# Performance work log

Measured on AMD Instinct MI355X. Metric: run time of the kernel, lower is better.

## Reference

```python
import jax, jax.numpy as jnp
import numpy as np

L = 2      # dec_num_layer
B = 32     # batch_size
T = 128    # block_len
H = 128    # dec_num_unit
F = 3      # code_rate_n / code_rate_k
D = 10


def _gru_cell(x, h, Wih, Whh, bih, bhh):
    # PyTorch GRU gate order: r, z, n
    gx = x @ Wih.T + bih
    gh = h @ Whh.T + bhh
    rx, zx, nx = jnp.split(gx, 3, axis=-1)
    rh, zh, nh = jnp.split(gh, 3, axis=-1)
    r = jax.nn.sigmoid(rx + rh)
    z = jax.nn.sigmoid(zx + zh)
    n = jnp.tanh(nx + r * nh)
    return (1.0 - z) * n + z * h


def _gru_stack(x, h, params):
    # x: [B, F], h: [L, B, H]; params: list of (Wih, Whh, bih, bhh) per layer
    hs = []
    inp = x
    for l, (Wih, Whh, bih, bhh) in enumerate(params):
        hl = _gru_cell(inp, h[l], Wih, Whh, bih, bhh)
        hs.append(hl)
        inp = hl
    return jnp.stack(hs), inp  # new hidden [L,B,H], top-layer output [B,H]


def _attend(h_raw, hist, i, attn_W, v_W, fc2_W, fc2_b):
    # h_raw: [L,B,H]; hist: [L,B,T,H]; growing-context attention with mask t<=i
    Ws, Wh = attn_W[:, :H], attn_W[:, H:]
    e = jnp.tanh((h_raw @ Ws.T)[:, :, None, :] + hist @ Wh.T)   # [L,B,T,H]
    logits = jnp.einsum('lbth,h->lbt', e, v_W[0])               # [L,B,T]
    mask = jnp.arange(T) <= i
    logits = jnp.where(mask[None, None, :], logits, -jnp.inf)
    a = jax.nn.softmax(logits, axis=-1)
    c = jnp.einsum('lbt,lbth->lbh', a, hist)                    # [L,B,H]
    return jnp.concatenate([c, h_raw], axis=-1) @ fc2_W.T + fc2_b


def _forward(received, params1, params2, attn_W, v_W, fc2_W, fc2_b, out_W, out_b):
    xs_seq = jnp.transpose(received, (1, 0, 2))  # [T,B,F]

    def step(carry, xs):
        h1, h2, hist1, hist2 = carry
        i, x = xs
        h1_raw, out1 = _gru_stack(x, h1, params1)
        h2_raw, out2 = _gru_stack(x, h2, params2)
        hist1 = hist1.at[:, :, i, :].set(h1_raw)
        hist2 = hist2.at[:, :, i, :].set(h2_raw)
        h1_att = _attend(h1_raw, hist1, i, attn_W, v_W, fc2_W, fc2_b)
        h2_att = _attend(h2_raw, hist2, i, attn_W, v_W, fc2_W, fc2_b)
        # torch skips the attention/fc2 update at step 0
        h1n = jnp.where(i > 0, h1_att, h1_raw)
        h2n = jnp.where(i > 0, h2_att, h2_raw)
        return (h1n, h2n, hist1, hist2), (out1, out2)

    z = jnp.zeros((L, B, H), dtype=received.dtype)
    zh = jnp.zeros((L, B, T, H), dtype=received.dtype)
    _, (o1, o2) = jax.lax.scan(step, (z, z, zh, zh), (jnp.arange(T), xs_seq))
    rnn1 = jnp.transpose(o1, (1, 0, 2))  # [B,T,H]
    rnn2 = jnp.transpose(o2, (1, 0, 2))

    idx = jnp.minimum(jnp.arange(T) + D, T - 1)
    rt_d = rnn2[:, idx, :]
    rnn_out = jnp.concatenate([rnn1, rt_d], axis=-1)            # [B,T,2H]
    dec = jnp.tanh(rnn_out @ out_W.T + out_b)                   # dec_act = tanh
    return jax.nn.sigmoid(dec)                                  # [B,T,1]


def setup_inputs() -> dict:
    key = jax.random.key(0)
    ks = iter(jax.random.split(key, 64))
    s = 0.05
    d = {"received": jax.random.normal(next(ks), (B, T, F), dtype=jnp.float32)}
    for dec in (1, 2):
        for l in range(L):
            inp = F if l == 0 else H
            d[f"Wih{dec}_{l}"] = jax.random.normal(next(ks), (3 * H, inp), dtype=jnp.float32) * s
            d[f"Whh{dec}_{l}"] = jax.random.normal(next(ks), (3 * H, H), dtype=jnp.float32) * s
            d[f"bih{dec}_{l}"] = jax.random.normal(next(ks), (3 * H,), dtype=jnp.float32) * s
            d[f"bhh{dec}_{l}"] = jax.random.normal(next(ks), (3 * H,), dtype=jnp.float32) * s
    d["attn_W"] = jax.random.normal(next(ks), (H, 2 * H), dtype=jnp.float32) * s
    d["v_W"] = jax.random.normal(next(ks), (1, H), dtype=jnp.float32) * s
    d["fc2_W"] = jax.random.normal(next(ks), (H, 2 * H), dtype=jnp.float32) * s
    d["fc2_b"] = jax.random.normal(next(ks), (H,), dtype=jnp.float32) * s
    d["out_W"] = jax.random.normal(next(ks), (1, 2 * H), dtype=jnp.float32) * s
    d["out_b"] = jax.random.normal(next(ks), (1,), dtype=jnp.float32) * s
    return d


def reference(received,
              Wih1_0, Whh1_0, bih1_0, bhh1_0, Wih1_1, Whh1_1, bih1_1, bhh1_1,
              Wih2_0, Whh2_0, bih2_0, bhh2_0, Wih2_1, Whh2_1, bih2_1, bhh2_1,
              attn_W, v_W, fc2_W, fc2_b, out_W, out_b):
    params1 = [(Wih1_0, Whh1_0, bih1_0, bhh1_0), (Wih1_1, Whh1_1, bih1_1, bhh1_1)]
    params2 = [(Wih2_0, Whh2_0, bih2_0, bhh2_0), (Wih2_1, Whh2_1, bih2_1, bhh2_1)]
    return _forward(received, params1, params2, attn_W, v_W, fc2_W, fc2_b, out_W, out_b)
```

## Files before the change

### kernel.cpp

```cpp
#include <hip/hip_runtime.h>

typedef _Float16 half_t;
typedef __attribute__((ext_vector_type(2))) _Float16 half2_t;

__device__ __forceinline__ half2_t bc2(unsigned int u){ return __builtin_bit_cast(half2_t, u); }
__device__ __forceinline__ int   bcI(half2_t v){ return __builtin_bit_cast(int, v); }
__device__ __forceinline__ half2_t bcH(int v){ return __builtin_bit_cast(half2_t, v); }
__device__ __forceinline__ float fdot2f(half2_t a, half2_t b, float c){
  return __builtin_amdgcn_fdot2(a, b, c, false);
}
__device__ __forceinline__ float rcp_f(float x){ return __builtin_amdgcn_rcpf(x); }
__device__ __forceinline__ float sigmoidf_(float x){ return rcp_f(1.0f+__expf(-x)); }
__device__ __forceinline__ float tanhf_(float x){ return 1.0f - 2.0f*rcp_f(__expf(2.0f*x)+1.0f); }

__device__ __forceinline__ float qxor1(float v){
  return __builtin_bit_cast(float, __builtin_amdgcn_mov_dpp(__builtin_bit_cast(int,v),0xB1,0xF,0xF,true));
}
__device__ __forceinline__ float qxor2(float v){
  return __builtin_bit_cast(float, __builtin_amdgcn_mov_dpp(__builtin_bit_cast(int,v),0x4E,0xF,0xF,true));
}
__device__ __forceinline__ float qsum4(float v){ v += qxor1(v); v += qxor2(v); return v; }

__device__ __forceinline__ void bar(){
  asm volatile("s_waitcnt lgkmcnt(0)\n\ts_barrier" ::: "memory");
}

__device__ __forceinline__ float dot32(const uint4* w, const uint4* x){
  float a=0.f,b=0.f,c=0.f,d=0.f;
  #pragma unroll
  for (int m=0;m<4;++m){
    a=fdot2f(bc2(w[m].x),bc2(x[m].x),a);
    b=fdot2f(bc2(w[m].y),bc2(x[m].y),b);
    c=fdot2f(bc2(w[m].z),bc2(x[m].z),c);
    d=fdot2f(bc2(w[m].w),bc2(x[m].w),d);
  }
  return (a+b)+(c+d);
}

__global__ void pack_k(const float* __restrict__ src, half_t* __restrict__ dst,
                       int R, int K, int ld, int coloff, int RT, int row_off){
  int idx = blockIdx.x*blockDim.x + threadIdx.x;
  if (idx >= R*K) return;
  int r = idx / K, k = idx - r*K;
  int kc = k >> 3, j = k & 7;
  dst[((size_t)kc*RT + row_off + r)*8 + j] = (half_t)src[(size_t)r*ld + coloff + k];
}

__launch_bounds__(512)
__global__ void gru_main(
    const float* __restrict__ received,
    const float* __restrict__ Wih0d0, const float* __restrict__ Wih0d1,
    const float* __restrict__ bx0d0, const float* __restrict__ bh0d0,
    const float* __restrict__ bx1d0, const float* __restrict__ bh1d0,
    const float* __restrict__ bx0d1, const float* __restrict__ bh0d1,
    const float* __restrict__ bx1d1, const float* __restrict__ bh1d1,
    const float* __restrict__ vW, const float* __restrict__ fc2b,
    const half_t* __restrict__ W0pack, const half_t* __restrict__ W1pack,
    const half_t* __restrict__ WsPack, const half_t* __restrict__ WhPack,
    const half_t* __restrict__ fc2Pack,
    half_t* __restrict__ o1h, half_t* __restrict__ o2h)
{
  const int dec = blockIdx.x >> 5;
  const int b   = blockIdx.x & 31;
  const int tid = threadIdx.x;
  const int q   = tid & 3;
  const int r   = tid >> 2;

  const float* bx0  = dec ? bx0d1 : bx0d0;
  const float* bh0  = dec ? bh0d1 : bh0d0;
  const float* bx1  = dec ? bx1d1 : bx1d0;
  const float* bh1  = dec ? bh1d1 : bh1d0;
  const float* Wih0 = dec ? Wih0d1 : Wih0d0;
  const half_t* W0  = W0pack + (size_t)dec*49152;
  const half_t* W1  = W1pack + (size_t)dec*98304;
  half_t* od = dec ? o2h : o1h;

  __shared__ __align__(16) half_t sh_hist[2][128*136];
  __shared__ __align__(16) half_t sh_histWh[2][128*136];
  __shared__ __align__(16) float  sh_gx[384];
  __shared__ __align__(16) float  sh_gh[384];
  __shared__ __align__(16) float  sh_g1x[384];
  __shared__ __align__(16) float  sh_g1h[384];
  __shared__ __align__(16) half_t sh_sWs16[2][128];
  __shared__ __align__(16) float  sh_probs[2][128];
  __shared__ __align__(16) float  sh_hatt32[2][128];
  __shared__ __align__(16) half_t sh_hatt_pk[2][128];
  __shared__ __align__(16) float  sh_hraw32[2][128];
  __shared__ __align__(16) half_t sh_hraw_pk[2][128];
  __shared__ __align__(16) half_t sh_fc2in[2][256];
  __shared__ __align__(16) half_t sh_vW16[128];

  float bA=0.f,bB=0.f,bC=0.f;
  if (q==0){ bA=bh0[r];     bB=bh1[r+128]; bC=bx1[r];     }
  else if (q==1){ bA=bh0[r+128]; bB=bh1[r+256]; bC=bx1[r+128]; }
  else if (q==2){ bA=bh0[r+256];                bC=bx1[r+256]; }
  else { bB=bh1[r]; }
  const float bF = fc2b[r];
  float wx0=0.f,wx1=0.f,wx2=0.f,wxw=0.f;
  if (tid < 384){ wx0=Wih0[tid*3]; wx1=Wih0[tid*3+1]; wx2=Wih0[tid*3+2]; wxw=bx0[tid]; }

  {
    uint4 z = make_uint4(0u,0u,0u,0u);
    uint4* ph = reinterpret_cast<uint4*>(&sh_hist[0][0]);
    uint4* pw = reinterpret_cast<uint4*>(&sh_histWh[0][0]);
    for (int j=tid; j<4352; j+=512){ ph[j]=z; pw[j]=z; }
  }
  if (tid < 256){ int l=tid>>7, rr=tid&127; sh_hatt32[l][rr]=0.f; sh_hatt_pk[l][rr]=(half_t)0.f; }
  if (tid < 128) sh_vW16[tid] = (half_t)vW[tid];
  bar();

  for (int i=0; i<128; ++i){
    {
      uint4 xa[4];
      #pragma unroll
      for (int m=0;m<4;++m) xa[m] = *reinterpret_cast<const uint4*>(&sh_hatt_pk[0][32*q+8*m]);
      float a0,a1,a2;
      {
        uint4 w[12];
        #pragma unroll
        for (int n=0;n<3;++n)
          #pragma unroll
          for (int m=0;m<4;++m)
            w[4*n+m] = *reinterpret_cast<const uint4*>(W0 + ((size_t)(4*q+m)*384 + r + 128*n)*8);
        a0 = dot32(&w[0],xa); a1 = dot32(&w[4],xa); a2 = dot32(&w[8],xa);
      }
      uint4 xb[4];
      #pragma unroll
      for (int m=0;m<4;++m) xb[m] = *reinterpret_cast<const uint4*>(&sh_hatt_pk[1][32*q+8*m]);
      float a3,a4,a5;
      {
        uint4 w[12];
        #pragma unroll
        for (int n=0;n<3;++n)
          #pragma unroll
          for (int m=0;m<4;++m)
            w[4*n+m] = *reinterpret_cast<const uint4*>(W1 + ((size_t)(4*q+m)*768 + 384 + r + 128*n)*8);
        a3 = dot32(&w[0],xb); a4 = dot32(&w[4],xb); a5 = dot32(&w[8],xb);
      }
      a0=qsum4(a0); a1=qsum4(a1); a2=qsum4(a2);
      a3=qsum4(a3); a4=qsum4(a4); a5=qsum4(a5);
      if      (q==0){ sh_gh[r]      = a0+bA; sh_g1h[r+128] = a4+bB; }
      else if (q==1){ sh_gh[r+128]  = a1+bA; sh_g1h[r+256] = a5+bB; }
      else if (q==2){ sh_gh[r+256]  = a2+bA; }
      else          { sh_g1h[r]     = a3+bB; }
      if (tid < 384){
        const float* xr = &received[((size_t)b*128+i)*3];
        sh_gx[tid] = wxw + wx0*xr[0] + wx1*xr[1] + wx2*xr[2];
      }
    }
    bar();
    if (tid < 128){
      float rr = sigmoidf_(sh_gx[tid]+sh_gh[tid]);
      float zz = sigmoidf_(sh_gx[128+tid]+sh_gh[128+tid]);
      float nn = tanhf_(sh_gx[256+tid] + rr*sh_gh[256+tid]);
      float h0 = (1.f-zz)*nn + zz*sh_hatt32[0][tid];
      sh_hraw32[0][tid]=h0;
      half_t hh=(half_t)h0;
      sh_hist[0][i*136 + ((tid>>3)^(i&15))*8 + (tid&7)] = hh;
      sh_hraw_pk[0][tid]=hh; sh_fc2in[0][128+tid]=hh;
    }
    bar();
    {
      uint4 xc[4];
      #pragma unroll
      for (int m=0;m<4;++m) xc[m] = *reinterpret_cast<const uint4*>(&sh_hraw_pk[0][32*q+8*m]);
      uint4 w[12];
      #pragma unroll
      for (int n=0;n<3;++n)
        #pragma unroll
        for (int m=0;m<4;++m)
          w[4*n+m] = *reinterpret_cast<const uint4*>(W1 + ((size_t)(4*q+m)*768 + r + 128*n)*8);
      float a0 = dot32(&w[0],xc), a1 = dot32(&w[4],xc), a2 = dot32(&w[8],xc);
      a0=qsum4(a0); a1=qsum4(a1); a2=qsum4(a2);
      if      (q==0) sh_g1x[r]     = a0+bC;
      else if (q==1) sh_g1x[r+128] = a1+bC;
      else if (q==2) sh_g1x[r+256] = a2+bC;
    }
    bar();
    if (tid < 128){
      float rr = sigmoidf_(sh_g1x[tid]+sh_g1h[tid]);
      float zz = sigmoidf_(sh_g1x[128+tid]+sh_g1h[128+tid]);
      float nn = tanhf_(sh_g1x[256+tid] + rr*sh_g1h[256+tid]);
      float h1 = (1.f-zz)*nn + zz*sh_hatt32[1][tid];
      sh_hraw32[1][tid]=h1;
      half_t hh=(half_t)h1;
      sh_hist[1][i*136 + ((tid>>3)^(i&15))*8 + (tid&7)] = hh;
      sh_hraw_pk[1][tid]=hh; sh_fc2in[1][128+tid]=hh;
      od[(size_t)(b*128+i)*128 + tid] = hh;
    }
    bar();
    {
      uint4 xa[4], xb[4], ws[4], wh[4];
      #pragma unroll
      for (int m=0;m<4;++m){
        xa[m] = *reinterpret_cast<const uint4*>(&sh_hraw_pk[0][32*q+8*m]);
        xb[m] = *reinterpret_cast<const uint4*>(&sh_hraw_pk[1][32*q+8*m]);
        ws[m] = *reinterpret_cast<const uint4*>(WsPack + ((size_t)(4*q+m)*128 + r)*8);
        wh[m] = *reinterpret_cast<const uint4*>(WhPack + ((size_t)(4*q+m)*128 + r)*8);
      }
      float sA0=qsum4(dot32(ws,xa));
      float sA1=qsum4(dot32(ws,xb));
      float sB0=qsum4(dot32(wh,xa));
      float sB1=qsum4(dot32(wh,xb));
      int phys = i*136 + ((r>>3)^(i&15))*8 + (r&7);
      if      (q==0) sh_sWs16[0][r] = (half_t)sA0;
      else if (q==1) sh_sWs16[1][r] = (half_t)sA1;
      else if (q==2) sh_histWh[0][phys] = (half_t)sB0;
      else           sh_histWh[1][phys] = (half_t)sB1;
    }
    bar();
    if (i > 0){
      {
        int h6=tid&1, t6=(tid>>1)&127, l6=tid>>8;
        if (t6 <= i){
          const half_t* hwrow = &sh_histWh[l6][t6*136];
          const half_t* swrow = &sh_sWs16[l6][64*h6];
          const half_t* vwrow = &sh_vW16[64*h6];
          int key = t6 & 15;
          float s = 0.f;
          #pragma unroll
          for (int m=0;m<8;++m){
            uint4 hw = *reinterpret_cast<const uint4*>(hwrow + (((8*h6+m)^key)*8));
            uint4 sw = *reinterpret_cast<const uint4*>(swrow + 8*m);
            uint4 vw = *reinterpret_cast<const uint4*>(vwrow + 8*m);
            half2_t h2,s2,v2;
            h2=bc2(hw.x); s2=bc2(sw.x); v2=bc2(vw.x);
            s += tanhf_((float)s2[0]+(float)h2[0])*(float)v2[0];
            s += tanhf_((float)s2[1]+(float)h2[1])*(float)v2[1];
            h2=bc2(hw.y); s2=bc2(sw.y); v2=bc2(vw.y);
            s += tanhf_((float)s2[0]+(float)h2[0])*(float)v2[0];
            s += tanhf_((float)s2[1]+(float)h2[1])*(float)v2[1];
            h2=bc2(hw.z); s2=bc2(sw.z); v2=bc2(vw.z);
            s += tanhf_((float)s2[0]+(float)h2[0])*(float)v2[0];
            s += tanhf_((float)s2[1]+(float)h2[1])*(float)v2[1];
            h2=bc2(hw.w); s2=bc2(sw.w); v2=bc2(vw.w);
            s += tanhf_((float)s2[0]+(float)h2[0])*(float)v2[0];
            s += tanhf_((float)s2[1]+(float)h2[1])*(float)v2[1];
          }
          s += qxor1(s);
          if (h6==0) sh_probs[l6][t6] = __expf(s - 4.0f);
        } else if ((tid&1)==0){
          sh_probs[tid>>8][(tid>>1)&127] = 0.f;
        }
      }
      bar();
      {
        int ts=tid&15, oc=(tid>>4)&15, l8=tid>>8;
        float c0=0.f,c1=0.f,c2=0.f,c3=0.f,c4=0.f,c5=0.f,c6=0.f,c7=0.f, ps=0.f;
        #pragma unroll
        for (int k=0;k<8;++k){
          int t = ts + 16*k;
          float p = sh_probs[l8][t];
          uint4 hv = *reinterpret_cast<const uint4*>(&sh_hist[l8][t*136 + ((oc^(t&15))*8)]);
          half2_t a=bc2(hv.x), e=bc2(hv.y), f=bc2(hv.z), g=bc2(hv.w);
          c0+=p*(float)a[0]; c1+=p*(float)a[1]; c2+=p*(float)e[0]; c3+=p*(float)e[1];
          c4+=p*(float)f[0]; c5+=p*(float)f[1]; c6+=p*(float)g[0]; c7+=p*(float)g[1];
          ps+=p;
        }
        c0+=qxor1(c0); c0+=qxor2(c0);  c1+=qxor1(c1); c1+=qxor2(c1);
        c2+=qxor1(c2); c2+=qxor2(c2);  c3+=qxor1(c3); c3+=qxor2(c3);
        c4+=qxor1(c4); c4+=qxor2(c4);  c5+=qxor1(c5); c5+=qxor2(c5);
        c6+=qxor1(c6); c6+=qxor2(c6);  c7+=qxor1(c7); c7+=qxor2(c7);
        ps+=qxor1(ps); ps+=qxor2(ps);
        half2_t p01={(half_t)c0,(half_t)c1}, p23={(half_t)c2,(half_t)c3};
        half2_t p45={(half_t)c4,(half_t)c5}, p67={(half_t)c6,(half_t)c7};
        p01 = p01 + bcH(__shfl_xor(bcI(p01),4)); p23 = p23 + bcH(__shfl_xor(bcI(p23),4));
        p45 = p45 + bcH(__shfl_xor(bcI(p45),4)); p67 = p67 + bcH(__shfl_xor(bcI(p67),4));
        ps += __shfl_xor(ps,4);
        p01 = p01 + bcH(__shfl_xor(bcI(p01),8)); p23 = p23 + bcH(__shfl_xor(bcI(p23),8));
        p45 = p45 + bcH(__shfl_xor(bcI(p45),8)); p67 = p67 + bcH(__shfl_xor(bcI(p67),8));
        ps += __shfl_xor(ps,8);
        if (ts==0){
          float inv = rcp_f(ps);
          half2_t o01={(half_t)((float)p01[0]*inv),(half_t)((float)p01[1]*inv)};
          half2_t o23={(half_t)((float)p23[0]*inv),(half_t)((float)p23[1]*inv)};
          half2_t o45={(half_t)((float)p45[0]*inv),(half_t)((float)p45[1]*inv)};
          half2_t o67={(half_t)((float)p67[0]*inv),(half_t)((float)p67[1]*inv)};
          *reinterpret_cast<uint4*>(&sh_fc2in[l8][oc*8]) =
              make_uint4((unsigned)bcI(o01),(unsigned)bcI(o23),(unsigned)bcI(o45),(unsigned)bcI(o67));
        }
      }
      bar();
      {
        float e0=0.f, e1=0.f;
        #pragma unroll
        for (int h=0; h<2; ++h){
          uint4 w[4], x0[4], x1[4];
          #pragma unroll
          for (int m=0;m<4;++m){
            int kc = 8*q + 4*h + m;
            w[m]  = *reinterpret_cast<const uint4*>(fc2Pack + ((size_t)kc*128 + r)*8);
            x0[m] = *reinterpret_cast<const uint4*>(&sh_fc2in[0][64*q + 32*h + 8*m]);
            x1[m] = *reinterpret_cast<const uint4*>(&sh_fc2in[1][64*q + 32*h + 8*m]);
          }
          e0 += dot32(w,x0);
          e1 += dot32(w,x1);
        }
        e0 = qsum4(e0); e1 = qsum4(e1);
        if      (q==0){ float v=e0+bF; sh_hatt32[0][r]=v; sh_hatt_pk[0][r]=(half_t)v; }
        else if (q==1){ float v=e1+bF; sh_hatt32[1][r]=v; sh_hatt_pk[1][r]=(half_t)v; }
      }
    } else {
      if (tid < 256){
        int l=tid>>7, row=tid&127;
        float hv = sh_hraw32[l][row];
        sh_hatt32[l][row]=hv; sh_hatt_pk[l][row]=(half_t)hv;
      }
    }
    bar();
  }
}

__global__ void out_kernel(const half_t* __restrict__ o1h, const half_t* __restrict__ o2h,
                           const float* __restrict__ outW, const float* __restrict__ outb,
                           float* __restrict__ dout){
  int tid = blockIdx.x*blockDim.x + threadIdx.x;
  int q = tid&3, job = tid>>2;
  int b = job>>7, t = job&127;
  int t2 = t+10; if (t2>127) t2=127;
  const half_t* r1 = o1h + (size_t)(b*128+t)*128;
  const half_t* r2 = o2h + (size_t)(b*128+t2)*128;
  float acc=0.f;
  for (int j=q*32; j<q*32+32; ++j) acc += outW[j]*(float)r1[j];
  for (int j=q*32; j<q*32+32; ++j) acc += outW[128+j]*(float)r2[j];
  acc += __shfl_xor(acc,1);
  acc += __shfl_xor(acc,2);
  if (q==0){
    float d = tanhf_(acc + outb[0]);
    dout[job] = rcp_f(1.f+__expf(-d));
  }
}

static inline void launch_pack(const void* src, half_t* dst, int R, int K, int ld,
                               int coloff, int RT, int row_off, hipStream_t s){
  int total = R*K;
  pack_k<<<(total+255)/256, 256, 0, s>>>((const float*)src, dst, R, K, ld, coloff, RT, row_off);
}

extern "C" void kernel_launch(void* const* d_in, const int* in_sizes, int n_in,
                              void* d_out, int out_size, void* d_ws, size_t ws_size,
                              hipStream_t stream) {
  const float* received = (const float*)d_in[0];
  const float* Wih1_0 = (const float*)d_in[1];
  const float* Whh1_0 = (const float*)d_in[2];
  const float* bih1_0 = (const float*)d_in[3];
  const float* bhh1_0 = (const float*)d_in[4];
  const float* Wih1_1 = (const float*)d_in[5];
  const float* Whh1_1 = (const float*)d_in[6];
  const float* bih1_1 = (const float*)d_in[7];
  const float* bhh1_1 = (const float*)d_in[8];
  const float* Wih2_0 = (const float*)d_in[9];
  const float* Whh2_0 = (const float*)d_in[10];
  const float* bih2_0 = (const float*)d_in[11];
  const float* bhh2_0 = (const float*)d_in[12];
  const float* Wih2_1 = (const float*)d_in[13];
  const float* Whh2_1 = (const float*)d_in[14];
  const float* bih2_1 = (const float*)d_in[15];
  const float* bhh2_1 = (const float*)d_in[16];
  const float* attn_W = (const float*)d_in[17];
  const float* v_W    = (const float*)d_in[18];
  const float* fc2_W  = (const float*)d_in[19];
  const float* fc2_b  = (const float*)d_in[20];
  const float* out_W  = (const float*)d_in[21];
  const float* out_b  = (const float*)d_in[22];

  half_t* ws = (half_t*)d_ws;
  half_t* W0pack  = ws + 0;
  half_t* W1pack  = ws + 98304;
  half_t* WsPack  = ws + 294912;
  half_t* WhPack  = ws + 311296;
  half_t* fc2Pack = ws + 327552;
  half_t* o1h     = ws + 360448;
  half_t* o2h     = ws + 884736;

  launch_pack(Whh1_0, W0pack,          384, 128, 128, 0, 384, 0, stream);
  launch_pack(Whh2_0, W0pack + 49152,  384, 128, 128, 0, 384, 0, stream);
  launch_pack(Wih1_1, W1pack,          384, 128, 128, 0, 768, 0, stream);
  launch_pack(Whh1_1, W1pack,          384, 128, 128, 0, 768, 384, stream);
  launch_pack(Wih2_1, W1pack + 98304,  384, 128, 128, 0, 768, 0, stream);
  launch_pack(Whh2_1, W1pack + 98304,  384, 128, 128, 0, 768, 384, stream);
  launch_pack(attn_W, WsPack,          128, 128, 256, 0,   128, 0, stream);
  launch_pack(attn_W, WhPack,          128, 128, 256, 128, 128, 0, stream);
  launch_pack(fc2_W,  fc2Pack,         128, 256, 256, 0,   128, 0, stream);

  gru_main<<<64, 512, 0, stream>>>(
      received,
      Wih1_0, Wih2_0,
      bih1_0, bhh1_0, bih1_1, bhh1_1,
      bih2_0, bhh2_0, bih2_1, bhh2_1,
      v_W, fc2_b,
      W0pack, W1pack, WsPack, WhPack, fc2Pack,
      o1h, o2h);

  out_kernel<<<64, 256, 0, stream>>>(o1h, o2h, out_W, out_b, (float*)d_out);
}
```

Measured before the change: 1.562 ms.

## Fold fc2 into attention history and fuse GRU gates to cut barriers

The fc2 projection is split algebraically. The context half is pre-applied to each history entry (histF = Wc·h), and the hidden half (Wh2·h_raw + b) is computed when h_raw is produced. Together these remove the per-step fc2 GEMV phase and one barrier. The GRU gate nonlinearities are now computed redundantly by all four quad lanes in registers, so the shared gx/gh/g1x/g1h buffers and two barriers are gone. The weighted history sum stays in fp32 instead of packed half shuffles. In exchange, each step does more redundant transcendental work and the layer-0 attention projections are loaded an extra time.

```diff
diff --git a/kernel.cpp b/kernel.cpp
--- a/kernel.cpp
+++ b/kernel.cpp
@@ -4,8 +4,6 @@
 typedef __attribute__((ext_vector_type(2))) _Float16 half2_t;
 
 __device__ __forceinline__ half2_t bc2(unsigned int u){ return __builtin_bit_cast(half2_t, u); }
-__device__ __forceinline__ int   bcI(half2_t v){ return __builtin_bit_cast(int, v); }
-__device__ __forceinline__ half2_t bcH(int v){ return __builtin_bit_cast(half2_t, v); }
 __device__ __forceinline__ float fdot2f(half2_t a, half2_t b, float c){
   return __builtin_amdgcn_fdot2(a, b, c, false);
 }
@@ -75,42 +73,41 @@
   const half_t* W1  = W1pack + (size_t)dec*98304;
   half_t* od = dec ? o2h : o1h;
 
-  __shared__ __align__(16) half_t sh_hist[2][128*136];
+  __shared__ __align__(16) half_t sh_histF[2][128*136];
   __shared__ __align__(16) half_t sh_histWh[2][128*136];
-  __shared__ __align__(16) float  sh_gx[384];
-  __shared__ __align__(16) float  sh_gh[384];
-  __shared__ __align__(16) float  sh_g1x[384];
-  __shared__ __align__(16) float  sh_g1h[384];
   __shared__ __align__(16) half_t sh_sWs16[2][128];
   __shared__ __align__(16) float  sh_probs[2][128];
   __shared__ __align__(16) float  sh_hatt32[2][128];
   __shared__ __align__(16) half_t sh_hatt_pk[2][128];
   __shared__ __align__(16) float  sh_hraw32[2][128];
   __shared__ __align__(16) half_t sh_hraw_pk[2][128];
-  __shared__ __align__(16) half_t sh_fc2in[2][256];
+  __shared__ __align__(16) float  sh_hF2[2][128];
   __shared__ __align__(16) half_t sh_vW16[128];
-
-  float bA=0.f,bB=0.f,bC=0.f;
-  if (q==0){ bA=bh0[r];     bB=bh1[r+128]; bC=bx1[r];     }
-  else if (q==1){ bA=bh0[r+128]; bB=bh1[r+256]; bC=bx1[r+128]; }
-  else if (q==2){ bA=bh0[r+256];                bC=bx1[r+256]; }
-  else { bB=bh1[r]; }
+  __shared__ __align__(16) float4 sh_Wx4[384];
+
+  const float bA0=bh0[r], bA1=bh0[r+128], bA2=bh0[r+256];
+  const float bB0=bh1[r], bB1=bh1[r+128], bB2=bh1[r+256];
+  const float bC0=bx1[r], bC1=bx1[r+128], bC2=bx1[r+256];
   const float bF = fc2b[r];
-  float wx0=0.f,wx1=0.f,wx2=0.f,wxw=0.f;
-  if (tid < 384){ wx0=Wih0[tid*3]; wx1=Wih0[tid*3+1]; wx2=Wih0[tid*3+2]; wxw=bx0[tid]; }
 
   {
     uint4 z = make_uint4(0u,0u,0u,0u);
-    uint4* ph = reinterpret_cast<uint4*>(&sh_hist[0][0]);
+    uint4* ph = reinterpret_cast<uint4*>(&sh_histF[0][0]);
     uint4* pw = reinterpret_cast<uint4*>(&sh_histWh[0][0]);
     for (int j=tid; j<4352; j+=512){ ph[j]=z; pw[j]=z; }
   }
   if (tid < 256){ int l=tid>>7, rr=tid&127; sh_hatt32[l][rr]=0.f; sh_hatt_pk[l][rr]=(half_t)0.f; }
   if (tid < 128) sh_vW16[tid] = (half_t)vW[tid];
+  if (tid < 384) sh_Wx4[tid] = make_float4(Wih0[tid*3], Wih0[tid*3+1], Wih0[tid*3+2], bx0[tid]);
   bar();
 
+  float g1h0=0.f, g1h1=0.f, g1h2=0.f;
+
   for (int i=0; i<128; ++i){
+    const int phys = i*136 + ((r>>3)^(i&15))*8 + (r&7);
     {
+      const float* xr = &received[((size_t)b*128+i)*3];
+      float xv0=xr[0], xv1=xr[1], xv2=xr[2];
       uint4 xa[4];
       #pragma unroll
       for (int m=0;m<4;++m) xa[m] = *reinterpret_cast<const uint4*>(&sh_hatt_pk[0][32*q+8*m]);
@@ -124,6 +121,7 @@
             w[4*n+m] = *reinterpret_cast<const uint4*>(W0 + ((size_t)(4*q+m)*384 + r + 128*n)*8);
         a0 = dot32(&w[0],xa); a1 = dot32(&w[4],xa); a2 = dot32(&w[8],xa);
       }
+      __builtin_amdgcn_sched_barrier(0);
       uint4 xb[4];
       #pragma unroll
       for (int m=0;m<4;++m) xb[m] = *reinterpret_cast<const uint4*>(&sh_hatt_pk[1][32*q+8*m]);
@@ -137,76 +135,89 @@
             w[4*n+m] = *reinterpret_cast<const uint4*>(W1 + ((size_t)(4*q+m)*768 + 384 + r + 128*n)*8);
         a3 = dot32(&w[0],xb); a4 = dot32(&w[4],xb); a5 = dot32(&w[8],xb);
       }
-      a0=qsum4(a0); a1=qsum4(a1); a2=qsum4(a2);
-      a3=qsum4(a3); a4=qsum4(a4); a5=qsum4(a5);
-      if      (q==0){ sh_gh[r]      = a0+bA; sh_g1h[r+128] = a4+bB; }
-      else if (q==1){ sh_gh[r+128]  = a1+bA; sh_g1h[r+256] = a5+bB; }
-      else if (q==2){ sh_gh[r+256]  = a2+bA; }
-      else          { sh_g1h[r]     = a3+bB; }
-      if (tid < 384){
-        const float* xr = &received[((size_t)b*128+i)*3];
-        sh_gx[tid] = wxw + wx0*xr[0] + wx1*xr[1] + wx2*xr[2];
-      }
-    }
-    bar();
-    if (tid < 128){
-      float rr = sigmoidf_(sh_gx[tid]+sh_gh[tid]);
-      float zz = sigmoidf_(sh_gx[128+tid]+sh_gh[128+tid]);
-      float nn = tanhf_(sh_gx[256+tid] + rr*sh_gh[256+tid]);
-      float h0 = (1.f-zz)*nn + zz*sh_hatt32[0][tid];
-      sh_hraw32[0][tid]=h0;
-      half_t hh=(half_t)h0;
-      sh_hist[0][i*136 + ((tid>>3)^(i&15))*8 + (tid&7)] = hh;
-      sh_hraw_pk[0][tid]=hh; sh_fc2in[0][128+tid]=hh;
+      a0=qsum4(a0)+bA0; a1=qsum4(a1)+bA1; a2=qsum4(a2)+bA2;
+      g1h0=qsum4(a3)+bB0; g1h1=qsum4(a4)+bB1; g1h2=qsum4(a5)+bB2;
+      float4 wxa=sh_Wx4[r], wxb=sh_Wx4[r+128], wxc=sh_Wx4[r+256];
+      float gxr = wxa.w + wxa.x*xv0 + wxa.y*xv1 + wxa.z*xv2;
+      float gxz = wxb.w + wxb.x*xv0 + wxb.y*xv1 + wxb.z*xv2;
+      float gxn = wxc.w + wxc.x*xv0 + wxc.y*xv1 + wxc.z*xv2;
+      float rr = sigmoidf_(gxr + a0);
+      float zz = sigmoidf_(gxz + a1);
+      float nn = tanhf_(gxn + rr*a2);
+      float h0 = (1.f-zz)*nn + zz*sh_hatt32[0][r];
+      if (q==0){ sh_hraw32[0][r]=h0; sh_hraw_pk[0][r]=(half_t)h0; }
     }
     bar();
     {
       uint4 xc[4];
       #pragma unroll
       for (int m=0;m<4;++m) xc[m] = *reinterpret_cast<const uint4*>(&sh_hraw_pk[0][32*q+8*m]);
-      uint4 w[12];
-      #pragma unroll
-      for (int n=0;n<3;++n)
-        #pragma unroll
-        for (int m=0;m<4;++m)
-          w[4*n+m] = *reinterpret_cast<const uint4*>(W1 + ((size_t)(4*q+m)*768 + r + 128*n)*8);
-      float a0 = dot32(&w[0],xc), a1 = dot32(&w[4],xc), a2 = dot32(&w[8],xc);
-      a0=qsum4(a0); a1=qsum4(a1); a2=qsum4(a2);
-      if      (q==0) sh_g1x[r]     = a0+bC;
-      else if (q==1) sh_g1x[r+128] = a1+bC;
-      else if (q==2) sh_g1x[r+256] = a2+bC;
-    }
-    bar();
-    if (tid < 128){
-      float rr = sigmoidf_(sh_g1x[tid]+sh_g1h[tid]);
-      float zz = sigmoidf_(sh_g1x[128+tid]+sh_g1h[128+tid]);
-      float nn = tanhf_(sh_g1x[256+tid] + rr*sh_g1h[256+tid]);
-      float h1 = (1.f-zz)*nn + zz*sh_hatt32[1][tid];
-      sh_hraw32[1][tid]=h1;
-      half_t hh=(half_t)h1;
-      sh_hist[1][i*136 + ((tid>>3)^(i&15))*8 + (tid&7)] = hh;
-      sh_hraw_pk[1][tid]=hh; sh_fc2in[1][128+tid]=hh;
-      od[(size_t)(b*128+i)*128 + tid] = hh;
+      float c0,c1,c2;
+      {
+        uint4 w[12];
+        #pragma unroll
+        for (int n=0;n<3;++n)
+          #pragma unroll
+          for (int m=0;m<4;++m)
+            w[4*n+m] = *reinterpret_cast<const uint4*>(W1 + ((size_t)(4*q+m)*768 + r + 128*n)*8);
+        c0 = dot32(&w[0],xc); c1 = dot32(&w[4],xc); c2 = dot32(&w[8],xc);
+      }
+      __builtin_amdgcn_sched_barrier(0);
+      float s0,hw0;
+      {
+        uint4 ws[4], wh[4];
+        #pragma unroll
+        for (int m=0;m<4;++m){
+          ws[m] = *reinterpret_cast<const uint4*>(WsPack + ((size_t)(4*q+m)*128 + r)*8);
+          wh[m] = *reinterpret_cast<const uint4*>(WhPack + ((size_t)(4*q+m)*128 + r)*8);
+        }
+        s0 = dot32(ws,xc); hw0 = dot32(wh,xc);
+      }
+      __builtin_amdgcn_sched_barrier(0);
+      float f0,f1;
+      {
+        uint4 fa[4], fb[4];
+        #pragma unroll
+        for (int m=0;m<4;++m){
+          fa[m] = *reinterpret_cast<const uint4*>(fc2Pack + ((size_t)(4*q+m)*128 + r)*8);
+          fb[m] = *reinterpret_cast<const uint4*>(fc2Pack + ((size_t)(16+4*q+m)*128 + r)*8);
+        }
+        f0 = dot32(fa,xc); f1 = dot32(fb,xc);
+      }
+      c0=qsum4(c0)+bC0; c1=qsum4(c1)+bC1; c2=qsum4(c2)+bC2;
+      s0=qsum4(s0); hw0=qsum4(hw0); f0=qsum4(f0); f1=qsum4(f1);
+      float rr = sigmoidf_(c0 + g1h0);
+      float zz = sigmoidf_(c1 + g1h1);
+      float nn = tanhf_(c2 + rr*g1h2);
+      float h1 = (1.f-zz)*nn + zz*sh_hatt32[1][r];
+      if (q==0){
+        sh_hraw32[1][r]=h1; half_t hh=(half_t)h1;
+        sh_hraw_pk[1][r]=hh; od[(size_t)(b*128+i)*128 + r]=hh;
+      } else if (q==1){ sh_histWh[0][phys]=(half_t)hw0; }
+      else if (q==2){ sh_histF[0][phys]=(half_t)f0; }
+      else { sh_sWs16[0][r]=(half_t)s0; sh_hF2[0][r]=f1+bF; }
     }
     bar();
     {
-      uint4 xa[4], xb[4], ws[4], wh[4];
+      uint4 xe[4];
+      #pragma unroll
+      for (int m=0;m<4;++m) xe[m] = *reinterpret_cast<const uint4*>(&sh_hraw_pk[1][32*q+8*m]);
+      uint4 ws[4], wh[4], fa[4], fb[4];
       #pragma unroll
       for (int m=0;m<4;++m){
-        xa[m] = *reinterpret_cast<const uint4*>(&sh_hraw_pk[0][32*q+8*m]);
-        xb[m] = *reinterpret_cast<const uint4*>(&sh_hraw_pk[1][32*q+8*m]);
         ws[m] = *reinterpret_cast<const uint4*>(WsPack + ((size_t)(4*q+m)*128 + r)*8);
         wh[m] = *reinterpret_cast<const uint4*>(WhPack + ((size_t)(4*q+m)*128 + r)*8);
-      }
-      float sA0=qsum4(dot32(ws,xa));
-      float sA1=qsum4(dot32(ws,xb));
-      float sB0=qsum4(dot32(wh,xa));
-      float sB1=qsum4(dot32(wh,xb));
-      int phys = i*136 + ((r>>3)^(i&15))*8 + (r&7);
-      if      (q==0) sh_sWs16[0][r] = (half_t)sA0;
-      else if (q==1) sh_sWs16[1][r] = (half_t)sA1;
-      else if (q==2) sh_histWh[0][phys] = (half_t)sB0;
-      else           sh_histWh[1][phys] = (half_t)sB1;
+        fa[m] = *reinterpret_cast<const uint4*>(fc2Pack + ((size_t)(4*q+m)*128 + r)*8);
+        fb[m] = *reinterpret_cast<const uint4*>(fc2Pack + ((size_t)(16+4*q+m)*128 + r)*8);
+      }
+      float s1  = qsum4(dot32(ws,xe));
+      float hw1 = qsum4(dot32(wh,xe));
+      float f0b = qsum4(dot32(fa,xe));
+      float f1b = qsum4(dot32(fb,xe));
+      if      (q==0) sh_sWs16[1][r]=(half_t)s1;
+      else if (q==1) sh_histWh[1][phys]=(half_t)hw1;
+      else if (q==2) sh_histF[1][phys]=(half_t)f0b;
+      else           sh_hF2[1][r]=f1b+bF;
     }
     bar();
     if (i > 0){
@@ -251,7 +262,7 @@
         for (int k=0;k<8;++k){
           int t = ts + 16*k;
           float p = sh_probs[l8][t];
-          uint4 hv = *reinterpret_cast<const uint4*>(&sh_hist[l8][t*136 + ((oc^(t&15))*8)]);
+          uint4 hv = *reinterpret_cast<const uint4*>(&sh_histF[l8][t*136 + ((oc^(t&15))*8)]);
           half2_t a=bc2(hv.x), e=bc2(hv.y), f=bc2(hv.z), g=bc2(hv.w);
           c0+=p*(float)a[0]; c1+=p*(float)a[1]; c2+=p*(float)e[0]; c3+=p*(float)e[1];
           c4+=p*(float)f[0]; c5+=p*(float)f[1]; c6+=p*(float)g[0]; c7+=p*(float)g[1];
@@ -262,43 +273,26 @@
         c4+=qxor1(c4); c4+=qxor2(c4);  c5+=qxor1(c5); c5+=qxor2(c5);
         c6+=qxor1(c6); c6+=qxor2(c6);  c7+=qxor1(c7); c7+=qxor2(c7);
         ps+=qxor1(ps); ps+=qxor2(ps);
-        half2_t p01={(half_t)c0,(half_t)c1}, p23={(half_t)c2,(half_t)c3};
-        half2_t p45={(half_t)c4,(half_t)c5}, p67={(half_t)c6,(half_t)c7};
-        p01 = p01 + bcH(__shfl_xor(bcI(p01),4)); p23 = p23 + bcH(__shfl_xor(bcI(p23),4));
-        p45 = p45 + bcH(__shfl_xor(bcI(p45),4)); p67 = p67 + bcH(__shfl_xor(bcI(p67),4));
-        ps += __shfl_xor(ps,4);
-        p01 = p01 + bcH(__shfl_xor(bcI(p01),8)); p23 = p23 + bcH(__shfl_xor(bcI(p23),8));
-        p45 = p45 + bcH(__shfl_xor(bcI(p45),8)); p67 = p67 + bcH(__shfl_xor(bcI(p67),8));
-        ps += __shfl_xor(ps,8);
+        c0+=__shfl_xor(c0,4); c1+=__shfl_xor(c1,4); c2+=__shfl_xor(c2,4); c3+=__shfl_xor(c3,4);
+        c4+=__shfl_xor(c4,4); c5+=__shfl_xor(c5,4); c6+=__shfl_xor(c6,4); c7+=__shfl_xor(c7,4);
+        ps+=__shfl_xor(ps,4);
+        c0+=__shfl_xor(c0,8); c1+=__shfl_xor(c1,8); c2+=__shfl_xor(c2,8); c3+=__shfl_xor(c3,8);
+        c4+=__shfl_xor(c4,8); c5+=__shfl_xor(c5,8); c6+=__shfl_xor(c6,8); c7+=__shfl_xor(c7,8);
+        ps+=__shfl_xor(ps,8);
         if (ts==0){
           float inv = rcp_f(ps);
-          half2_t o01={(half_t)((float)p01[0]*inv),(half_t)((float)p01[1]*inv)};
-          half2_t o23={(half_t)((float)p23[0]*inv),(half_t)((float)p23[1]*inv)};
-          half2_t o45={(half_t)((float)p45[0]*inv),(half_t)((float)p45[1]*inv)};
-          half2_t o67={(half_t)((float)p67[0]*inv),(half_t)((float)p67[1]*inv)};
-          *reinterpret_cast<uint4*>(&sh_fc2in[l8][oc*8]) =
-              make_uint4((unsigned)bcI(o01),(unsigned)bcI(o23),(unsigned)bcI(o45),(unsigned)bcI(o67));
-        }
-      }
-      bar();
-      {
-        float e0=0.f, e1=0.f;
-        #pragma unroll
-        for (int h=0; h<2; ++h){
-          uint4 w[4], x0[4], x1[4];
-          #pragma unroll
-          for (int m=0;m<4;++m){
-            int kc = 8*q + 4*h + m;
-            w[m]  = *reinterpret_cast<const uint4*>(fc2Pack + ((size_t)kc*128 + r)*8);
-            x0[m] = *reinterpret_cast<const uint4*>(&sh_fc2in[0][64*q + 32*h + 8*m]);
-            x1[m] = *reinterpret_cast<const uint4*>(&sh_fc2in[1][64*q + 32*h + 8*m]);
-          }
-          e0 += dot32(w,x0);
-          e1 += dot32(w,x1);
-        }
-        e0 = qsum4(e0); e1 = qsum4(e1);
-        if      (q==0){ float v=e0+bF; sh_hatt32[0][r]=v; sh_hatt_pk[0][r]=(half_t)v; }
-        else if (q==1){ float v=e1+bF; sh_hatt32[1][r]=v; sh_hatt_pk[1][r]=(half_t)v; }
+          const float* hf = &sh_hF2[l8][8*oc];
+          float v0=hf[0]+c0*inv, v1=hf[1]+c1*inv, v2=hf[2]+c2*inv, v3=hf[3]+c3*inv;
+          float v4=hf[4]+c4*inv, v5=hf[5]+c5*inv, v6=hf[6]+c6*inv, v7=hf[7]+c7*inv;
+          float* ho = &sh_hatt32[l8][8*oc];
+          *reinterpret_cast<float4*>(ho)   = make_float4(v0,v1,v2,v3);
+          *reinterpret_cast<float4*>(ho+4) = make_float4(v4,v5,v6,v7);
+          half2_t o01={(half_t)v0,(half_t)v1}, o23={(half_t)v2,(half_t)v3};
+          half2_t o45={(half_t)v4,(half_t)v5}, o67={(half_t)v6,(half_t)v7};
+          *reinterpret_cast<uint4*>(&sh_hatt_pk[l8][8*oc]) =
+              make_uint4((unsigned)__builtin_bit_cast(int,o01),(unsigned)__builtin_bit_cast(int,o23),
+                         (unsigned)__builtin_bit_cast(int,o45),(unsigned)__builtin_bit_cast(int,o67));
+        }
       }
     } else {
       if (tid < 256){
```

After: 2.319 ms. 1.48x slower.

## Adapt attention scoring parallelism to context length and skip masked history work

Applied to the files above, without the earlier changes.

The attention score phase now splits each timestep's 128-wide dot across 8, 4 or 2 lanes depending on how many timesteps are valid. Early steps therefore spread over more threads instead of leaving most idle. The context accumulation loop only visits history chunks up to the current step. fc2 weights are prefetched into registers before the barrier so the global load overlaps the context reduction. Other changes: the input-projection weights move to shared memory to free registers, partial sums are reduced in fp32 instead of fp16 shuffles, and a sched_barrier splits the two GEMV halves. The trade-off is more code paths, higher register pressure from the prefetched weights, and a non-unrolled loop.

```diff
diff --git a/kernel.cpp b/kernel.cpp
--- a/kernel.cpp
+++ b/kernel.cpp
@@ -4,8 +4,6 @@
 typedef __attribute__((ext_vector_type(2))) _Float16 half2_t;
 
 __device__ __forceinline__ half2_t bc2(unsigned int u){ return __builtin_bit_cast(half2_t, u); }
-__device__ __forceinline__ int   bcI(half2_t v){ return __builtin_bit_cast(int, v); }
-__device__ __forceinline__ half2_t bcH(int v){ return __builtin_bit_cast(half2_t, v); }
 __device__ __forceinline__ float fdot2f(half2_t a, half2_t b, float c){
   return __builtin_amdgcn_fdot2(a, b, c, false);
 }
@@ -35,6 +33,49 @@
     d=fdot2f(bc2(w[m].w),bc2(x[m].w),d);
   }
   return (a+b)+(c+d);
+}
+
+template<int L>
+__device__ __forceinline__ void phase6(int i, int tid,
+    const half_t* shWh, const half_t* sWs0, const half_t* sWs1,
+    const half_t* vw, float* probs0, float* probs1)
+{
+  const int sub = tid & (L-1);
+  const int pid = tid / L;
+  const int t6  = (L==2) ? (pid & 127) : (L==4) ? (pid & 63) : (pid & 31);
+  const int l6  = (L==2) ? (pid >> 7)  : (L==4) ? (pid >> 6) : (pid >> 5);
+  if (t6 <= i){
+    const half_t* hwrow = shWh + (size_t)l6*(128*136) + t6*136;
+    const half_t* swrow = l6 ? sWs1 : sWs0;
+    const int M  = 16/L;
+    const int m0 = M*sub;
+    const int key = t6 & 15;
+    float s = 0.f;
+    #pragma unroll
+    for (int mm=0; mm<M; ++mm){
+      int m = m0+mm;
+      uint4 hw = *reinterpret_cast<const uint4*>(hwrow + ((m^key)*8));
+      uint4 sw = *reinterpret_cast<const uint4*>(swrow + 8*m);
+      uint4 vv = *reinterpret_cast<const uint4*>(vw + 8*m);
+      half2_t h2,s2,v2;
+      h2=bc2(hw.x); s2=bc2(sw.x); v2=bc2(vv.x);
+      s += tanhf_((float)s2[0]+(float)h2[0])*(float)v2[0];
+      s += tanhf_((float)s2[1]+(float)h2[1])*(float)v2[1];
+      h2=bc2(hw.y); s2=bc2(sw.y); v2=bc2(vv.y);
+      s += tanhf_((float)s2[0]+(float)h2[0])*(float)v2[0];
+      s += tanhf_((float)s2[1]+(float)h2[1])*(float)v2[1];
+      h2=bc2(hw.z); s2=bc2(sw.z); v2=bc2(vv.z);
+      s += tanhf_((float)s2[0]+(float)h2[0])*(float)v2[0];
+      s += tanhf_((float)s2[1]+(float)h2[1])*(float)v2[1];
+      h2=bc2(hw.w); s2=bc2(sw.w); v2=bc2(vv.w);
+      s += tanhf_((float)s2[0]+(float)h2[0])*(float)v2[0];
+      s += tanhf_((float)s2[1]+(float)h2[1])*(float)v2[1];
+    }
+    s += qxor1(s);
+    if (L>=4) s += qxor2(s);
+    if (L>=8) s += __shfl_xor(s,4);
+    if (sub==0) (l6 ? probs1 : probs0)[t6] = __expf(s - 4.0f);
+  }
 }
 
 __global__ void pack_k(const float* __restrict__ src, half_t* __restrict__ dst,
@@ -89,6 +130,7 @@
   __shared__ __align__(16) half_t sh_hraw_pk[2][128];
   __shared__ __align__(16) half_t sh_fc2in[2][256];
   __shared__ __align__(16) half_t sh_vW16[128];
+  __shared__ __align__(16) float4 sh_Wx4[384];
 
   float bA=0.f,bB=0.f,bC=0.f;
   if (q==0){ bA=bh0[r];     bB=bh1[r+128]; bC=bx1[r];     }
@@ -96,8 +138,6 @@
   else if (q==2){ bA=bh0[r+256];                bC=bx1[r+256]; }
   else { bB=bh1[r]; }
   const float bF = fc2b[r];
-  float wx0=0.f,wx1=0.f,wx2=0.f,wxw=0.f;
-  if (tid < 384){ wx0=Wih0[tid*3]; wx1=Wih0[tid*3+1]; wx2=Wih0[tid*3+2]; wxw=bx0[tid]; }
 
   {
     uint4 z = make_uint4(0u,0u,0u,0u);
@@ -107,6 +147,7 @@
   }
   if (tid < 256){ int l=tid>>7, rr=tid&127; sh_hatt32[l][rr]=0.f; sh_hatt_pk[l][rr]=(half_t)0.f; }
   if (tid < 128) sh_vW16[tid] = (half_t)vW[tid];
+  if (tid < 384) sh_Wx4[tid] = make_float4(Wih0[tid*3], Wih0[tid*3+1], Wih0[tid*3+2], bx0[tid]);
   bar();
 
   for (int i=0; i<128; ++i){
@@ -124,6 +165,7 @@
             w[4*n+m] = *reinterpret_cast<const uint4*>(W0 + ((size_t)(4*q+m)*384 + r + 128*n)*8);
         a0 = dot32(&w[0],xa); a1 = dot32(&w[4],xa); a2 = dot32(&w[8],xa);
       }
+      __builtin_amdgcn_sched_barrier(0);
       uint4 xb[4];
       #pragma unroll
       for (int m=0;m<4;++m) xb[m] = *reinterpret_cast<const uint4*>(&sh_hatt_pk[1][32*q+8*m]);
@@ -145,7 +187,8 @@
       else          { sh_g1h[r]     = a3+bB; }
       if (tid < 384){
         const float* xr = &received[((size_t)b*128+i)*3];
-        sh_gx[tid] = wxw + wx0*xr[0] + wx1*xr[1] + wx2*xr[2];
+        float4 wx = sh_Wx4[tid];
+        sh_gx[tid] = wx.w + wx.x*xr[0] + wx.y*xr[1] + wx.z*xr[2];
       }
     }
     bar();
@@ -210,45 +253,20 @@
     }
     bar();
     if (i > 0){
-      {
-        int h6=tid&1, t6=(tid>>1)&127, l6=tid>>8;
-        if (t6 <= i){
-          const half_t* hwrow = &sh_histWh[l6][t6*136];
-          const half_t* swrow = &sh_sWs16[l6][64*h6];
-          const half_t* vwrow = &sh_vW16[64*h6];
-          int key = t6 & 15;
-          float s = 0.f;
-          #pragma unroll
-          for (int m=0;m<8;++m){
-            uint4 hw = *reinterpret_cast<const uint4*>(hwrow + (((8*h6+m)^key)*8));
-            uint4 sw = *reinterpret_cast<const uint4*>(swrow + 8*m);
-            uint4 vw = *reinterpret_cast<const uint4*>(vwrow + 8*m);
-            half2_t h2,s2,v2;
-            h2=bc2(hw.x); s2=bc2(sw.x); v2=bc2(vw.x);
-            s += tanhf_((float)s2[0]+(float)h2[0])*(float)v2[0];
-            s += tanhf_((float)s2[1]+(float)h2[1])*(float)v2[1];
-            h2=bc2(hw.y); s2=bc2(sw.y); v2=bc2(vw.y);
-            s += tanhf_((float)s2[0]+(float)h2[0])*(float)v2[0];
-            s += tanhf_((float)s2[1]+(float)h2[1])*(float)v2[1];
-            h2=bc2(hw.z); s2=bc2(sw.z); v2=bc2(vw.z);
-            s += tanhf_((float)s2[0]+(float)h2[0])*(float)v2[0];
-            s += tanhf_((float)s2[1]+(float)h2[1])*(float)v2[1];
-            h2=bc2(hw.w); s2=bc2(sw.w); v2=bc2(vw.w);
-            s += tanhf_((float)s2[0]+(float)h2[0])*(float)v2[0];
-            s += tanhf_((float)s2[1]+(float)h2[1])*(float)v2[1];
-          }
-          s += qxor1(s);
-          if (h6==0) sh_probs[l6][t6] = __expf(s - 4.0f);
-        } else if ((tid&1)==0){
-          sh_probs[tid>>8][(tid>>1)&127] = 0.f;
-        }
-      }
+      if (i < 32)      phase6<8>(i, tid, &sh_histWh[0][0], &sh_sWs16[0][0], &sh_sWs16[1][0], &sh_vW16[0], &sh_probs[0][0], &sh_probs[1][0]);
+      else if (i < 64) phase6<4>(i, tid, &sh_histWh[0][0], &sh_sWs16[0][0], &sh_sWs16[1][0], &sh_vW16[0], &sh_probs[0][0], &sh_probs[1][0]);
+      else             phase6<2>(i, tid, &sh_histWh[0][0], &sh_sWs16[0][0], &sh_sWs16[1][0], &sh_vW16[0], &sh_probs[0][0], &sh_probs[1][0]);
+      if (tid < 256){ int l=tid>>7, t=tid&127; if (t > i) sh_probs[l][t] = 0.f; }
       bar();
+      uint4 wE[8];
+      #pragma unroll
+      for (int c=0;c<8;++c)
+        wE[c] = *reinterpret_cast<const uint4*>(fc2Pack + ((size_t)(8*q+c)*128 + r)*8);
       {
         int ts=tid&15, oc=(tid>>4)&15, l8=tid>>8;
         float c0=0.f,c1=0.f,c2=0.f,c3=0.f,c4=0.f,c5=0.f,c6=0.f,c7=0.f, ps=0.f;
-        #pragma unroll
-        for (int k=0;k<8;++k){
+        int kmax = (i>>4)+1;
+        for (int k=0;k<kmax;++k){
           int t = ts + 16*k;
           float p = sh_probs[l8][t];
           uint4 hv = *reinterpret_cast<const uint4*>(&sh_hist[l8][t*136 + ((oc^(t&15))*8)]);
@@ -262,22 +280,21 @@
         c4+=qxor1(c4); c4+=qxor2(c4);  c5+=qxor1(c5); c5+=qxor2(c5);
         c6+=qxor1(c6); c6+=qxor2(c6);  c7+=qxor1(c7); c7+=qxor2(c7);
         ps+=qxor1(ps); ps+=qxor2(ps);
-        half2_t p01={(half_t)c0,(half_t)c1}, p23={(half_t)c2,(half_t)c3};
-        half2_t p45={(half_t)c4,(half_t)c5}, p67={(half_t)c6,(half_t)c7};
-        p01 = p01 + bcH(__shfl_xor(bcI(p01),4)); p23 = p23 + bcH(__shfl_xor(bcI(p23),4));
-        p45 = p45 + bcH(__shfl_xor(bcI(p45),4)); p67 = p67 + bcH(__shfl_xor(bcI(p67),4));
-        ps += __shfl_xor(ps,4);
-        p01 = p01 + bcH(__shfl_xor(bcI(p01),8)); p23 = p23 + bcH(__shfl_xor(bcI(p23),8));
-        p45 = p45 + bcH(__shfl_xor(bcI(p45),8)); p67 = p67 + bcH(__shfl_xor(bcI(p67),8));
-        ps += __shfl_xor(ps,8);
+        c0+=__shfl_xor(c0,4); c1+=__shfl_xor(c1,4); c2+=__shfl_xor(c2,4); c3+=__shfl_xor(c3,4);
+        c4+=__shfl_xor(c4,4); c5+=__shfl_xor(c5,4); c6+=__shfl_xor(c6,4); c7+=__shfl_xor(c7,4);
+        ps+=__shfl_xor(ps,4);
+        c0+=__shfl_xor(c0,8); c1+=__shfl_xor(c1,8); c2+=__shfl_xor(c2,8); c3+=__shfl_xor(c3,8);
+        c4+=__shfl_xor(c4,8); c5+=__shfl_xor(c5,8); c6+=__shfl_xor(c6,8); c7+=__shfl_xor(c7,8);
+        ps+=__shfl_xor(ps,8);
         if (ts==0){
           float inv = rcp_f(ps);
-          half2_t o01={(half_t)((float)p01[0]*inv),(half_t)((float)p01[1]*inv)};
-          half2_t o23={(half_t)((float)p23[0]*inv),(half_t)((float)p23[1]*inv)};
-          half2_t o45={(half_t)((float)p45[0]*inv),(half_t)((float)p45[1]*inv)};
-          half2_t o67={(half_t)((float)p67[0]*inv),(half_t)((float)p67[1]*inv)};
+          half2_t o01={(half_t)(c0*inv),(half_t)(c1*inv)};
+          half2_t o23={(half_t)(c2*inv),(half_t)(c3*inv)};
+          half2_t o45={(half_t)(c4*inv),(half_t)(c5*inv)};
+          half2_t o67={(half_t)(c6*inv),(half_t)(c7*inv)};
           *reinterpret_cast<uint4*>(&sh_fc2in[l8][oc*8]) =
-              make_uint4((unsigned)bcI(o01),(unsigned)bcI(o23),(unsigned)bcI(o45),(unsigned)bcI(o67));
+              make_uint4((unsigned)__builtin_bit_cast(int,o01),(unsigned)__builtin_bit_cast(int,o23),
+                         (unsigned)__builtin_bit_cast(int,o45),(unsigned)__builtin_bit_cast(int,o67));
         }
       }
       bar();
@@ -285,16 +302,14 @@
         float e0=0.f, e1=0.f;
         #pragma unroll
         for (int h=0; h<2; ++h){
-          uint4 w[4], x0[4], x1[4];
+          uint4 x0[4], x1[4];
           #pragma unroll
           for (int m=0;m<4;++m){
-            int kc = 8*q + 4*h + m;
-            w[m]  = *reinterpret_cast<const uint4*>(fc2Pack + ((size_t)kc*128 + r)*8);
             x0[m] = *reinterpret_cast<const uint4*>(&sh_fc2in[0][64*q + 32*h + 8*m]);
             x1[m] = *reinterpret_cast<const uint4*>(&sh_fc2in[1][64*q + 32*h + 8*m]);
           }
-          e0 += dot32(w,x0);
-          e1 += dot32(w,x1);
+          e0 += dot32(&wE[4*h],x0);
+          e1 += dot32(&wE[4*h],x1);
         }
         e0 = qsum4(e0); e1 = qsum4(e1);
         if      (q==0){ float v=e0+bF; sh_hatt32[0][r]=v; sh_hatt_pk[0][r]=(half_t)v; }
```

Result: faster. 1.407 ms (-10.0%).
